# Kernel optimization log

Measured on AMD Instinct MI355X. Metric: run time of the kernel, lower is better.

## Reference

```python
import jax, jax.numpy as jnp
import numpy as np

HID = 64
NUM_LAYERS = 2
EPS = 1e-5


def _layernorm(x, g, b):
    mu = jnp.mean(x, axis=-1, keepdims=True)
    var = jnp.mean(jnp.square(x - mu), axis=-1, keepdims=True)
    return (x - mu) * jax.lax.rsqrt(var + EPS) * g + b


def _mlp(x, w1, b1, g, beta, w2, b2):
    # Linear -> LayerNorm -> ReLU -> Linear (torch Linear: x @ W.T + b)
    h = x @ w1.T + b1
    h = jax.nn.relu(_layernorm(h, g, beta))
    return h @ w2.T + b2


def _gru(x, h, wih, whh, bih, bhh):
    # PyTorch GRUCell semantics
    gi = x @ wih.T + bih
    gh = h @ whh.T + bhh
    ir, iz, inn = jnp.split(gi, 3, axis=-1)
    hr, hz, hn = jnp.split(gh, 3, axis=-1)
    r = jax.nn.sigmoid(ir + hr)
    z = jax.nn.sigmoid(iz + hz)
    n = jnp.tanh(inn + r * hn)
    return (1.0 - z) * n + z * h


def setup_inputs() -> dict:
    key = jax.random.key(0)
    ks = iter(jax.random.split(key, 64))
    s = 0.05

    def rn(shape):
        return jax.random.normal(next(ks), shape, dtype=jnp.float32) * s

    B, M, K1 = 32, 256, 128
    inp = {
        'hybrid_input': jax.random.normal(next(ks), (B, M, K1, 4), dtype=jnp.float32),
        'hidden_state': jnp.zeros((B, HID), dtype=jnp.float32),
        # input encoder
        'enc_w1': rn((HID, 4)), 'enc_b1': rn((HID,)),
        'enc_g': jnp.ones((HID,), jnp.float32), 'enc_beta': jnp.zeros((HID,), jnp.float32),
        'enc_w2': rn((HID, HID)), 'enc_b2': rn((HID,)),
        # per-layer, per-side (axis0=layer, axis1=[row,col]) params
        'l_w1': rn((NUM_LAYERS, 2, HID, HID)), 'l_b1': rn((NUM_LAYERS, 2, HID)),
        'l_g': jnp.ones((NUM_LAYERS, 2, HID), jnp.float32), 'l_beta': jnp.zeros((NUM_LAYERS, 2, HID), jnp.float32),
        'l_w2': rn((NUM_LAYERS, 2, HID, HID)), 'l_b2': rn((NUM_LAYERS, 2, HID)),
        'l_gwih': rn((NUM_LAYERS, 2, 3 * HID, HID)), 'l_gwhh': rn((NUM_LAYERS, 2, 3 * HID, HID)),
        'l_gbih': rn((NUM_LAYERS, 2, 3 * HID)), 'l_gbhh': rn((NUM_LAYERS, 2, 3 * HID)),
        # top-level GRU
        'g_wih': rn((3 * HID, HID)), 'g_whh': rn((3 * HID, HID)),
        'g_bih': rn((3 * HID,)), 'g_bhh': rn((3 * HID,)),
        # head: Linear(2H->H) -> ReLU -> Linear(H->1)
        'head_w1': rn((HID, 2 * HID)), 'head_b1': rn((HID,)),
        'head_w2': rn((1, HID)), 'head_b2': rn((1,)),
    }
    return inp


def reference(hybrid_input, hidden_state, enc_w1, enc_b1, enc_g, enc_beta, enc_w2, enc_b2,
              l_w1, l_b1, l_g, l_beta, l_w2, l_b2, l_gwih, l_gwhh, l_gbih, l_gbhh,
              g_wih, g_whh, g_bih, g_bhh, head_w1, head_b1, head_w2, head_b2):
    # input encoder
    x = _mlp(hybrid_input, enc_w1, enc_b1, enc_g, enc_beta, enc_w2, enc_b2)

    for l in range(NUM_LAYERS):
        # row pass: max over axis 2 (K+1)
        row_max = jnp.max(x, axis=2, keepdims=True)
        upd = _mlp(x - row_max, l_w1[l, 0], l_b1[l, 0], l_g[l, 0], l_beta[l, 0], l_w2[l, 0], l_b2[l, 0])
        x = _gru(upd, x, l_gwih[l, 0], l_gwhh[l, 0], l_gbih[l, 0], l_gbhh[l, 0])
        # col pass: max over axis 1 (M)
        col_max = jnp.max(x, axis=1, keepdims=True)
        upd = _mlp(x - col_max, l_w1[l, 1], l_b1[l, 1], l_g[l, 1], l_beta[l, 1], l_w2[l, 1], l_b2[l, 1])
        x = _gru(upd, x, l_gwih[l, 1], l_gwhh[l, 1], l_gbih[l, 1], l_gbhh[l, 1])

    B, M, K1, h = x.shape
    global_feat = jnp.max(x.reshape(B, M * K1, h), axis=1)  # (B, H)
    new_hidden = _gru(global_feat, hidden_state, g_wih, g_whh, g_bih, g_bhh)

    h_exp = jnp.broadcast_to(new_hidden[:, None, None, :], (B, M, K1, h))
    combined = jnp.concatenate([x, h_exp], axis=-1)  # (B, M, K1, 2H)
    hh = jax.nn.relu(combined @ head_w1.T + head_b1)
    logits = (hh @ head_w2.T + head_b2)[..., 0]  # (B, M, K1)
    return logits, new_hidden
```

## Files before the change

kernel.cpp:

```cpp
#include <hip/hip_runtime.h>
#include <math.h>

typedef unsigned int u32;
typedef unsigned short u16;
typedef __attribute__((ext_vector_type(4))) float f32x4;
typedef __attribute__((ext_vector_type(8))) short s16x8;

#define NTOT 1048576
#define SWZ(n, col) ((col) ^ (((n) & 7) << 4))

__device__ __forceinline__ float bflo(u32 v) { return __uint_as_float(v << 16); }
__device__ __forceinline__ float bfhi(u32 v) { return __uint_as_float(v & 0xffff0000u); }
__device__ __forceinline__ u32 rndbf(float f) {
  u32 u = __float_as_uint(f);
  return u + 0x7fffu + ((u >> 16) & 1u);
}
__device__ __forceinline__ u32 pk2(float a, float b) {
  return __builtin_amdgcn_perm(rndbf(b), rndbf(a), 0x07060302u);
}
__device__ __forceinline__ float sigm(float x) {
  return __builtin_amdgcn_rcpf(1.0f + __expf(-x));
}
__device__ __forceinline__ float tanh_f(float x) {
  float e = __expf(2.0f * x);
  return 1.0f - 2.0f * __builtin_amdgcn_rcpf(e + 1.0f);
}
__device__ __forceinline__ float relu(float x) { return fmaxf(x, 0.0f); }

__device__ __forceinline__ void gemmG(const ushort* __restrict__ gA,
                                      const unsigned char* L, int boff,
                                      int ws, int l, int lq, int lr,
                                      f32x4 acc[4]) {
  s16x8 a0 = *(const s16x8*)(gA + ((ws * 128 + l) << 3));
  s16x8 a1 = *(const s16x8*)(gA + ((ws * 128 + 64 + l) << 3));
  const int c0 = (lq << 4) ^ ((lr & 7) << 4);
  const unsigned char* Bp = L + boff + lr * 128;
#pragma unroll
  for (int nt = 0; nt < 4; ++nt) {
    s16x8 b0 = *(const s16x8*)(Bp + nt * 2048 + c0);
    s16x8 b1 = *(const s16x8*)(Bp + nt * 2048 + (c0 ^ 64));
    acc[nt] = __builtin_amdgcn_mfma_f32_16x16x32_bf16(a0, b0, acc[nt], 0, 0, 0);
    acc[nt] = __builtin_amdgcn_mfma_f32_16x16x32_bf16(a1, b1, acc[nt], 0, 0, 0);
  }
}

__device__ __forceinline__ void gemmG2(const ushort* __restrict__ gA,
                                       const unsigned char* L, int boff,
                                       int ws, int nh, int l, int lq, int lr,
                                       f32x4 acc[4]) {
  s16x8 a0 = *(const s16x8*)(gA + ((ws * 128 + l) << 3));
  s16x8 a1 = *(const s16x8*)(gA + ((ws * 128 + 64 + l) << 3));
  const int c0 = (lq << 4) ^ ((lr & 7) << 4);
  const unsigned char* Bp = L + boff + nh * 8192 + lr * 128;
#pragma unroll
  for (int nt = 0; nt < 4; ++nt) {
    s16x8 b0 = *(const s16x8*)(Bp + nt * 2048 + c0);
    s16x8 b1 = *(const s16x8*)(Bp + nt * 2048 + (c0 ^ 64));
    acc[nt] = __builtin_amdgcn_mfma_f32_16x16x32_bf16(a0, b0, acc[nt], 0, 0, 0);
    acc[nt] = __builtin_amdgcn_mfma_f32_16x16x32_bf16(a1, b1, acc[nt], 0, 0, 0);
  }
}

__device__ __forceinline__ void binit(f32x4 acc[4], float x, float y, float z, float w) {
  f32x4 v; v[0] = x; v[1] = y; v[2] = z; v[3] = w;
#pragma unroll
  for (int nt = 0; nt < 4; ++nt) acc[nt] = v;
}

__global__ void diag_kernel(float* out, float v) { out[0] = v; }

__global__ __launch_bounds__(256) void prep_kernel(
    const float* __restrict__ enc_w2, const float* __restrict__ head_w1,
    const float* __restrict__ l_w1, const float* __restrict__ l_w2,
    const float* __restrict__ l_gwih, const float* __restrict__ l_gwhh,
    ushort* __restrict__ gwF) {
  const int id = blockIdx.x;
  const int t = threadIdx.x;
  const float* src;
  int ld = 64;
  if (id == 0)      { src = enc_w2; }
  else if (id == 1) { src = head_w1; ld = 128; }
  else if (id < 6)  { src = l_w1 + (id - 2) * 4096; }
  else if (id < 10) { src = l_w2 + (id - 6) * 4096; }
  else if (id < 22) { int q = id - 10; src = l_gwih + (q / 3) * 12288 + (q % 3) * 4096; }
  else              { int q = id - 22; src = l_gwhh + (q / 3) * 12288 + (q % 3) * 4096; }
  uint4* dst = (uint4*)(gwF + (size_t)id * 4096);
#pragma unroll
  for (int i = 0; i < 2; ++i) {
    int ch = i * 256 + t;
    int q = ch & 63;
    int g = ch >> 6;
    int j = (g >> 1) * 16 + (q & 15);
    int k = (g & 1) * 32 + (q >> 4) * 8;
    const float* s = src + (size_t)j * ld + k;
    float4 f0 = *(const float4*)(s);
    float4 f1 = *(const float4*)(s + 4);
    uint4 o;
    o.x = pk2(f0.x, f0.y); o.y = pk2(f0.z, f0.w);
    o.z = pk2(f1.x, f1.y); o.w = pk2(f1.z, f1.w);
    dst[ch] = o;
  }
}

__global__ __launch_bounds__(512) void encoder_kernel(
    const float4* __restrict__ hyb, ushort* __restrict__ xG,
    const ushort* __restrict__ gwF, const float* __restrict__ enc_w1,
    const float* __restrict__ b1, const float* __restrict__ gg,
    const float* __restrict__ be, const float* __restrict__ b2,
    float* __restrict__ rmOut) {
  __shared__ __align__(16) unsigned char L[17920];
  const int t = threadIdx.x;
  const int w = t >> 6, l = t & 63, lq = l >> 4, lr = l & 15;
  const int ws = w & 3, nh = w >> 2;
  const int gbase = blockIdx.x * 128;
  const int j0 = ws * 16 + lq * 4;

  if (t < 256) ((float*)(L + 16384))[t] = enc_w1[t];
  __syncthreads();

  {
    const int n = t >> 2, part = t & 3;
    float4 iv = hyb[gbase + n];
    const float* W1 = (const float*)(L + 16384);
    float h[16];
#pragma unroll
    for (int jj = 0; jj < 16; ++jj) {
      int j = part * 16 + jj;
      float4 wr = *(const float4*)(W1 + j * 4);
      h[jj] = b1[j] + wr.x * iv.x + wr.y * iv.y + wr.z * iv.z + wr.w * iv.w;
    }
    float s = 0.f, q = 0.f;
#pragma unroll
    for (int jj = 0; jj < 16; ++jj) { s += h[jj]; q += h[jj] * h[jj]; }
    s += __shfl_xor(s, 1); q += __shfl_xor(q, 1);
    s += __shfl_xor(s, 2); q += __shfl_xor(q, 2);
    float mean = s * (1.f / 64.f);
    float rstd = rsqrtf(q * (1.f / 64.f) - mean * mean + 1e-5f);
    u32 pk[8];
#pragma unroll
    for (int jj = 0; jj < 16; jj += 2) {
      int j = part * 16 + jj;
      float v0 = relu((h[jj] - mean) * rstd * gg[j] + be[j]);
      float v1 = relu((h[jj + 1] - mean) * rstd * gg[j + 1] + be[j + 1]);
      pk[jj >> 1] = pk2(v0, v1);
    }
    *(uint4*)(L + n * 128 + SWZ(n, part * 32))      = make_uint4(pk[0], pk[1], pk[2], pk[3]);
    *(uint4*)(L + n * 128 + SWZ(n, part * 32 + 16)) = make_uint4(pk[4], pk[5], pk[6], pk[7]);
  }
  __syncthreads();

  float4 vb2 = *(const float4*)(b2 + j0);
  f32x4 acc[4];
  binit(acc, vb2.x, vb2.y, vb2.z, vb2.w);
  gemmG2(gwF, L, 0, ws, nh, l, lq, lr, acc);
  {
    ushort* xout = xG + (size_t)gbase * 64;
#pragma unroll
    for (int nt = 0; nt < 4; ++nt) {
      int n = nh * 64 + nt * 16 + lr;
      *(uint2*)(xout + (size_t)n * 64 + j0) =
          make_uint2(pk2(acc[nt][0], acc[nt][1]), pk2(acc[nt][2], acc[nt][3]));
    }
  }
  {
    float mt[4];
#pragma unroll
    for (int r = 0; r < 4; ++r)
      mt[r] = fmaxf(fmaxf(acc[0][r], acc[1][r]), fmaxf(acc[2][r], acc[3][r]));
#pragma unroll
    for (int m = 1; m < 16; m <<= 1)
#pragma unroll
      for (int r = 0; r < 4; ++r) mt[r] = fmaxf(mt[r], __shfl_xor(mt[r], m));
    if (lr == 0) {
      float4 v; v.x = mt[0]; v.y = mt[1]; v.z = mt[2]; v.w = mt[3];
      *(float4*)(L + 17408 + (nh * 64 + j0) * 4) = v;
    }
  }
  __syncthreads();
  if (t < 64) {
    const float* R = (const float*)(L + 17408);
    float v = fmaxf(R[t], R[64 + t]);
    rmOut[(size_t)(blockIdx.x * 2 + 0) * 64 + t] = v;
    rmOut[(size_t)(blockIdx.x * 2 + 1) * 64 + t] = v;
  }
}

#define PXL 0
#define PP  8192
#define PMV 16384
#define PU  16384
#define PRED 24576

__global__ __launch_bounds__(256, 5) void pass_kernel(
    ushort* __restrict__ xG, const ushort* __restrict__ gwF,
    const float* __restrict__ rmP, const ushort* __restrict__ cmB, int mode,
    int s_w1, int s_w2, int s_ih0, int s_hh0,
    const float* __restrict__ b1, const float* __restrict__ b2,
    const float* __restrict__ gg, const float* __restrict__ be,
    const float* __restrict__ bih, const float* __restrict__ bhh,
    float* __restrict__ rmOut) {
  __shared__ __align__(16) unsigned char L[26624];
  const int t = threadIdx.x;
  const int ws = t >> 6, l = t & 63, lq = l >> 4, lr = l & 15;
  const int gbase = blockIdx.x * 64;
  const int j0 = ws * 16 + lq * 4;
  const int colb = ws * 32 + lq * 8;
  const int rowp = (gbase >> 7) * 2;
  const int b = gbase >> 15;
  const int k1b = gbase & 127;

  const ushort* Aw1 = gwF + (size_t)s_w1 * 4096;
  const ushort* Aw2 = gwF + (size_t)s_w2 * 4096;
  const ushort* Ai0 = gwF + (size_t)s_ih0 * 4096;
  const ushort* Ai1 = Ai0 + 4096;
  const ushort* Ai2 = Ai1 + 4096;
  const ushort* Ah0 = gwF + (size_t)s_hh0 * 4096;
  const ushort* Ah1 = Ah0 + 4096;
  const ushort* Ah2 = Ah1 + 4096;

  {
    const uint4* xrow = (const uint4*)(xG + (size_t)gbase * 64);
    const int c = t & 7;
    uint4 mvo;
    if (mode == 0) {
      const float* r0 = rmP + (size_t)rowp * 64 + c * 8;
      float mv[8];
#pragma unroll
      for (int q = 0; q < 8; ++q) mv[q] = -fmaxf(r0[q], r0[64 + q]);
      mvo.x = pk2(mv[0], mv[1]); mvo.y = pk2(mv[2], mv[3]);
      mvo.z = pk2(mv[4], mv[5]); mvo.w = pk2(mv[6], mv[7]);
    }
#pragma unroll
    for (int i = 0; i < 2; ++i) {
      int flat = i * 256 + t; int n = flat >> 3;
      *(uint4*)(L + PXL + n * 128 + SWZ(n, c * 16)) = xrow[(size_t)n * 8 + c];
      uint4 o = mvo;
      if (mode == 1)
        o = ((const uint4*)cmB)[(size_t)(b * 128 + k1b + n) * 8 + c];
      *(uint4*)(L + PMV + n * 128 + SWZ(n, c * 16)) = o;
    }
  }
  __syncthreads();

  f32x4 acc[4];
  { float4 v = *(const float4*)(b1 + j0); binit(acc, v.x, v.y, v.z, v.w); }
  gemmG(Aw1, L, PXL, ws, l, lq, lr, acc);
  gemmG(Aw1, L, PMV, ws, l, lq, lr, acc);
#pragma unroll
  for (int nt = 0; nt < 4; ++nt) {
    float s = acc[nt][0] + acc[nt][1] + acc[nt][2] + acc[nt][3];
    float q = acc[nt][0] * acc[nt][0] + acc[nt][1] * acc[nt][1] +
              acc[nt][2] * acc[nt][2] + acc[nt][3] * acc[nt][3];
    s += __shfl_xor(s, 16); q += __shfl_xor(q, 16);
    s += __shfl_xor(s, 32); q += __shfl_xor(q, 32);
    if (lq == 0)
      *(float2*)(L + PRED + (ws * 64 + nt * 16 + lr) * 8) = make_float2(s, q);
  }
  __syncthreads();
  {
    float4 vg = *(const float4*)(gg + j0);
    float4 vbe = *(const float4*)(be + j0);
    float gv[4] = {vg.x, vg.y, vg.z, vg.w};
    float bv[4] = {vbe.x, vbe.y, vbe.z, vbe.w};
#pragma unroll
    for (int nt = 0; nt < 4; ++nt) {
      int np = nt * 16 + lr;
      float ss = 0.f, qq = 0.f;
#pragma unroll
      for (int wv = 0; wv < 4; ++wv) {
        float2 pr = *(const float2*)(L + PRED + (wv * 64 + np) * 8);
        ss += pr.x; qq += pr.y;
      }
      float mean = ss * (1.f / 64.f);
      float rstd = rsqrtf(qq * (1.f / 64.f) - mean * mean + 1e-5f);
      float h_[4];
#pragma unroll
      for (int r = 0; r < 4; ++r) h_[r] = relu((acc[nt][r] - mean) * rstd * gv[r] + bv[r]);
      *(uint2*)(L + PP + np * 128 + SWZ(np, colb)) =
          make_uint2(pk2(h_[0], h_[1]), pk2(h_[2], h_[3]));
    }
  }
  __syncthreads();
  __builtin_amdgcn_sched_barrier(0);

  { float4 v = *(const float4*)(b2 + j0); binit(acc, v.x, v.y, v.z, v.w); }
  gemmG(Aw2, L, PP, ws, l, lq, lr, acc);
#pragma unroll
  for (int nt = 0; nt < 4; ++nt) {
    int n = nt * 16 + lr;
    *(uint2*)(L + PU + n * 128 + SWZ(n, colb)) =
        make_uint2(pk2(acc[nt][0], acc[nt][1]), pk2(acc[nt][2], acc[nt][3]));
  }
  __builtin_amdgcn_sched_barrier(0);

  f32x4 ah[4];
  { float4 v = *(const float4*)(bhh + 128 + j0); binit(ah, v.x, v.y, v.z, v.w); }
  gemmG(Ah2, L, PXL, ws, l, lq, lr, ah);
  __syncthreads();
  __builtin_amdgcn_sched_barrier(0);

  f32x4 ar[4];
  { float4 vi = *(const float4*)(bih + j0);
    float4 vh = *(const float4*)(bhh + j0);
    binit(ar, vi.x + vh.x, vi.y + vh.y, vi.z + vh.z, vi.w + vh.w); }
  gemmG(Ai0, L, PU, ws, l, lq, lr, ar);
  gemmG(Ah0, L, PXL, ws, l, lq, lr, ar);
  __builtin_amdgcn_sched_barrier(0);

  f32x4 an[4];
  { float4 v = *(const float4*)(bih + 128 + j0);
    float bv[4] = {v.x, v.y, v.z, v.w};
#pragma unroll
    for (int nt = 0; nt < 4; ++nt)
#pragma unroll
      for (int r = 0; r < 4; ++r)
        an[nt][r] = bv[r] + sigm(ar[nt][r]) * ah[nt][r];
  }
  gemmG(Ai2, L, PU, ws, l, lq, lr, an);
  __builtin_amdgcn_sched_barrier(0);

  f32x4 az[4];
  { float4 vi = *(const float4*)(bih + 64 + j0);
    float4 vh = *(const float4*)(bhh + 64 + j0);
    binit(az, vi.x + vh.x, vi.y + vh.y, vi.z + vh.z, vi.w + vh.w); }
  gemmG(Ai1, L, PU, ws, l, lq, lr, az);
  gemmG(Ah1, L, PXL, ws, l, lq, lr, az);

  float xn[4][4];
#pragma unroll
  for (int nt = 0; nt < 4; ++nt) {
    int n = nt * 16 + lr;
    uint2 xo = *(const uint2*)(L + PXL + n * 128 + SWZ(n, colb));
    float xv[4] = {bflo(xo.x), bfhi(xo.x), bflo(xo.y), bfhi(xo.y)};
#pragma unroll
    for (int r = 0; r < 4; ++r) {
      float nn = tanh_f(an[nt][r]);
      float zz = sigm(az[nt][r]);
      xn[nt][r] = nn + zz * (xv[r] - nn);
    }
  }
  {
    ushort* xout = xG + (size_t)gbase * 64;
#pragma unroll
    for (int nt = 0; nt < 4; ++nt) {
      int n = nt * 16 + lr;
      *(uint2*)(xout + (size_t)n * 64 + j0) =
          make_uint2(pk2(xn[nt][0], xn[nt][1]), pk2(xn[nt][2], xn[nt][3]));
    }
  }
  {
    float mt[4];
#pragma unroll
    for (int r = 0; r < 4; ++r)
      mt[r] = fmaxf(fmaxf(xn[0][r], xn[1][r]), fmaxf(xn[2][r], xn[3][r]));
#pragma unroll
    for (int m = 1; m < 16; m <<= 1)
#pragma unroll
      for (int r = 0; r < 4; ++r) mt[r] = fmaxf(mt[r], __shfl_xor(mt[r], m));
    if (lr == 0) {
      float4 v; v.x = mt[0]; v.y = mt[1]; v.z = mt[2]; v.w = mt[3];
      *(float4*)(rmOut + (size_t)blockIdx.x * 64 + j0) = v;
    }
  }
}

__global__ __launch_bounds__(256) void colmax_kernel(const ushort* __restrict__ xG,
                                                     ushort* __restrict__ cmB) {
  const int t = threadIdx.x;
  const int b = blockIdx.x >> 4, kg = blockIdx.x & 15;
  const int col = t & 31, k1 = kg * 8 + (t >> 5);
  const u32* xu = (const u32*)xG;
  float m0 = -INFINITY, m1 = -INFINITY;
  for (int m = 0; m < 256; ++m) {
    size_t node = ((size_t)(b * 256 + m)) * 128 + k1;
    u32 v = xu[node * 32 + col];
    m0 = fmaxf(m0, bflo(v)); m1 = fmaxf(m1, bfhi(v));
  }
  ((u32*)cmB)[((size_t)(b * 128 + k1)) * 32 + col] = pk2(-m0, -m1);
}

__global__ __launch_bounds__(64) void topgru_kernel(
    const float* __restrict__ rm, const float* __restrict__ hs,
    const float* __restrict__ gwih, const float* __restrict__ gwhh,
    const float* __restrict__ gbih, const float* __restrict__ gbhh,
    float* __restrict__ nh, float* __restrict__ outTail) {
  __shared__ float gf[64], h0[64];
  const int b = blockIdx.x, j = threadIdx.x;
  float g0 = -INFINITY, g1 = -INFINITY, g2 = -INFINITY, g3 = -INFINITY;
  const float* base = rm + (size_t)b * 512 * 64 + j;
  for (int r = 0; r < 512; r += 4) {
    g0 = fmaxf(g0, base[(r + 0) * 64]);
    g1 = fmaxf(g1, base[(r + 1) * 64]);
    g2 = fmaxf(g2, base[(r + 2) * 64]);
    g3 = fmaxf(g3, base[(r + 3) * 64]);
  }
  gf[j] = fmaxf(fmaxf(g0, g1), fmaxf(g2, g3));
  h0[j] = hs[b * 64 + j];
  __syncthreads();
  float gi[3], gh[3];
#pragma unroll
  for (int g = 0; g < 3; ++g) {
    float s = gbih[g * 64 + j];
    const float* wr = gwih + (g * 64 + j) * 64;
    for (int k = 0; k < 64; ++k) s += wr[k] * gf[k];
    gi[g] = s;
  }
#pragma unroll
  for (int g = 0; g < 3; ++g) {
    float s = gbhh[g * 64 + j];
    const float* wr = gwhh + (g * 64 + j) * 64;
    for (int k = 0; k < 64; ++k) s += wr[k] * h0[k];
    gh[g] = s;
  }
  float rr = sigm(gi[0] + gh[0]);
  float zz = sigm(gi[1] + gh[1]);
  float nn = tanh_f(gi[2] + rr * gh[2]);
  float val = (1.0f - zz) * nn + zz * h0[j];
  nh[b * 64 + j] = val;
  outTail[b * 64 + j] = val;
}

__global__ __launch_bounds__(64) void hc_kernel(const float* __restrict__ nh,
                                                const float* __restrict__ hw1,
                                                const float* __restrict__ hb1,
                                                float* __restrict__ hc) {
  __shared__ float h0[64];
  const int b = blockIdx.x, j = threadIdx.x;
  h0[j] = nh[b * 64 + j];
  __syncthreads();
  float s = hb1[j];
  const float* wr = hw1 + j * 128 + 64;
  for (int k = 0; k < 64; ++k) s += wr[k] * h0[k];
  hc[b * 64 + j] = s;
}

__global__ __launch_bounds__(512) void head_kernel(
    const ushort* __restrict__ xG, const ushort* __restrict__ gwF,
    const float* __restrict__ hc, const float* __restrict__ hw2,
    const float* __restrict__ hb2, float* __restrict__ out) {
  __shared__ __align__(16) unsigned char L[18432];
  const int t = threadIdx.x;
  const int w = t >> 6, l = t & 63, lq = l >> 4, lr = l & 15;
  const int ws = w & 3, nh = w >> 2;
  const int gbase = blockIdx.x * 128;
  const int b = gbase >> 15;
  const int j0 = ws * 16 + lq * 4;

  { const uint4* xrow = (const uint4*)(xG + (size_t)gbase * 64);
#pragma unroll
    for (int i = 0; i < 2; ++i) {
      int flat = i * 512 + t; int n = flat >> 3, c = flat & 7;
      *(uint4*)(L + n * 128 + SWZ(n, c * 16)) = xrow[(size_t)n * 8 + c];
    } }
  __syncthreads();

  float4 vhc = *(const float4*)(hc + b * 64 + j0);
  f32x4 acc[4];
  binit(acc, vhc.x, vhc.y, vhc.z, vhc.w);
  gemmG2(gwF + 4096, L, 0, ws, nh, l, lq, lr, acc);

  float4 w2v = *(const float4*)(hw2 + j0);
  float w2a[4] = {w2v.x, w2v.y, w2v.z, w2v.w};
#pragma unroll
  for (int nt = 0; nt < 4; ++nt) {
    float p = 0.f;
#pragma unroll
    for (int r = 0; r < 4; ++r) p += w2a[r] * relu(acc[nt][r]);
    p += __shfl_xor(p, 16);
    p += __shfl_xor(p, 32);
    if (lq == 0) ((float*)(L + 16384))[(nh * 4 + ws) * 64 + nt * 16 + lr] = p;
  }
  __syncthreads();
  if (t < 128) {
    const float* red = (const float*)(L + 16384) + (t >> 6) * 256 + (t & 63);
    out[gbase + t] = red[0] + red[64] + red[128] + red[192] + hb2[0];
  }
}

extern "C" void kernel_launch(void* const* d_in, const int* in_sizes, int n_in,
                              void* d_out, int out_size, void* d_ws, size_t ws_size,
                              hipStream_t stream) {
  const float* hybrid   = (const float*)d_in[0];
  const float* hidden   = (const float*)d_in[1];
  const float* enc_w1   = (const float*)d_in[2];
  const float* enc_b1   = (const float*)d_in[3];
  const float* enc_g    = (const float*)d_in[4];
  const float* enc_beta = (const float*)d_in[5];
  const float* enc_w2   = (const float*)d_in[6];
  const float* enc_b2   = (const float*)d_in[7];
  const float* l_w1     = (const float*)d_in[8];
  const float* l_b1     = (const float*)d_in[9];
  const float* l_g      = (const float*)d_in[10];
  const float* l_beta   = (const float*)d_in[11];
  const float* l_w2     = (const float*)d_in[12];
  const float* l_b2     = (const float*)d_in[13];
  const float* l_gwih   = (const float*)d_in[14];
  const float* l_gwhh   = (const float*)d_in[15];
  const float* l_gbih   = (const float*)d_in[16];
  const float* l_gbhh   = (const float*)d_in[17];
  const float* g_wih    = (const float*)d_in[18];
  const float* g_whh    = (const float*)d_in[19];
  const float* g_bih    = (const float*)d_in[20];
  const float* g_bhh    = (const float*)d_in[21];
  const float* head_w1  = (const float*)d_in[22];
  const float* head_b1  = (const float*)d_in[23];
  const float* head_w2  = (const float*)d_in[24];
  const float* head_b2  = (const float*)d_in[25];

  char* p = (char*)d_ws;
  size_t off = 0;
  auto carve = [&](size_t bytes) { void* r = p + off; off = (off + bytes + 255) & ~255ULL; return r; };
  ushort* xG  = (ushort*)carve((size_t)NTOT * 64 * 2);
  ushort* gwF = (ushort*)carve(34 * 4096 * 2);
  float*  rmA = (float*)carve((size_t)16384 * 64 * 4);
  float*  rmB = (float*)carve((size_t)16384 * 64 * 4);
  ushort* cmB = (ushort*)carve((size_t)32 * 128 * 64 * 2);
  float*  nh  = (float*)carve(2048 * 4);
  float*  hcb = (float*)carve(2048 * 4);

  if (ws_size < off) {
    diag_kernel<<<1, 1, 0, stream>>>((float*)d_out, 1.0f + (float)ws_size * 1e-9f);
    return;
  }

  prep_kernel<<<34, 256, 0, stream>>>(enc_w2, head_w1, l_w1, l_w2, l_gwih, l_gwhh, gwF);
  encoder_kernel<<<8192, 512, 0, stream>>>((const float4*)hybrid, xG, gwF, enc_w1,
                                           enc_b1, enc_g, enc_beta, enc_b2, rmA);

  float* rmRead = rmA;
  float* rmWrite = rmB;
  for (int lyr = 0; lyr < 2; ++lyr) {
    for (int s = 0; s < 2; ++s) {
      const int m = lyr * 2 + s;
      if (s == 1) colmax_kernel<<<512, 256, 0, stream>>>(xG, cmB);
      pass_kernel<<<16384, 256, 0, stream>>>(
          xG, gwF, rmRead, cmB, s,
          2 + m, 6 + m, 10 + 3 * m, 22 + 3 * m,
          l_b1 + m * 64, l_b2 + m * 64, l_g + m * 64, l_beta + m * 64,
          l_gbih + m * 192, l_gbhh + m * 192, rmWrite);
      float* tmp = rmRead; rmRead = rmWrite; rmWrite = tmp;
    }
  }

  topgru_kernel<<<32, 64, 0, stream>>>(rmRead, hidden, g_wih, g_whh, g_bih, g_bhh,
                                       nh, (float*)d_out + 1048576);
  hc_kernel<<<32, 64, 0, stream>>>(nh, head_w1, head_b1, hcb);
  head_kernel<<<8192, 512, 0, stream>>>(xG, gwF, hcb, head_w2, head_b2, (float*)d_out);
}
```

Baseline: 764.2 us.

## Load MFMA B operands from global into registers instead of staging through LDS

The pass and head kernels now read x fragments straight from global memory into per-lane registers in MFMA B-operand layout and reuse them across the W1 and the three GRU hidden GEMMs, instead of staging x (and the max vector) in swizzled LDS. In row mode the broadcast row-max term is reduced to a single MFMA pair instead of a full 64-column GEMM, since all columns share the same vector. This cuts LDS use per block (the pass kernel's launch bound drops from 5 to 4 blocks per SIMD) and removes a staging barrier. The cost is more VGPR pressure, and the final GRU blend rereads x from global.

```diff
diff --git a/kernel.cpp b/kernel.cpp
--- a/kernel.cpp
+++ b/kernel.cpp
@@ -18,6 +18,12 @@
 __device__ __forceinline__ u32 pk2(float a, float b) {
   return __builtin_amdgcn_perm(rndbf(b), rndbf(a), 0x07060302u);
 }
+__device__ __forceinline__ s16x8 pack8(const float m[8]) {
+  union { u32 w[4]; s16x8 v; } cv;
+  cv.w[0] = pk2(m[0], m[1]); cv.w[1] = pk2(m[2], m[3]);
+  cv.w[2] = pk2(m[4], m[5]); cv.w[3] = pk2(m[6], m[7]);
+  return cv.v;
+}
 __device__ __forceinline__ float sigm(float x) {
   return __builtin_amdgcn_rcpf(1.0f + __expf(-x));
 }
@@ -26,6 +32,18 @@
   return 1.0f - 2.0f * __builtin_amdgcn_rcpf(e + 1.0f);
 }
 __device__ __forceinline__ float relu(float x) { return fmaxf(x, 0.0f); }
+
+__device__ __forceinline__ void gemmR(const ushort* __restrict__ gA,
+                                      const s16x8 bf[8],
+                                      int ws, int l, f32x4 acc[4]) {
+  s16x8 a0 = *(const s16x8*)(gA + ((ws * 128 + l) << 3));
+  s16x8 a1 = *(const s16x8*)(gA + ((ws * 128 + 64 + l) << 3));
+#pragma unroll
+  for (int nt = 0; nt < 4; ++nt) {
+    acc[nt] = __builtin_amdgcn_mfma_f32_16x16x32_bf16(a0, bf[nt * 2 + 0], acc[nt], 0, 0, 0);
+    acc[nt] = __builtin_amdgcn_mfma_f32_16x16x32_bf16(a1, bf[nt * 2 + 1], acc[nt], 0, 0, 0);
+  }
+}
 
 __device__ __forceinline__ void gemmG(const ushort* __restrict__ gA,
                                       const unsigned char* L, int boff,
@@ -35,23 +53,6 @@
   s16x8 a1 = *(const s16x8*)(gA + ((ws * 128 + 64 + l) << 3));
   const int c0 = (lq << 4) ^ ((lr & 7) << 4);
   const unsigned char* Bp = L + boff + lr * 128;
-#pragma unroll
-  for (int nt = 0; nt < 4; ++nt) {
-    s16x8 b0 = *(const s16x8*)(Bp + nt * 2048 + c0);
-    s16x8 b1 = *(const s16x8*)(Bp + nt * 2048 + (c0 ^ 64));
-    acc[nt] = __builtin_amdgcn_mfma_f32_16x16x32_bf16(a0, b0, acc[nt], 0, 0, 0);
-    acc[nt] = __builtin_amdgcn_mfma_f32_16x16x32_bf16(a1, b1, acc[nt], 0, 0, 0);
-  }
-}
-
-__device__ __forceinline__ void gemmG2(const ushort* __restrict__ gA,
-                                       const unsigned char* L, int boff,
-                                       int ws, int nh, int l, int lq, int lr,
-                                       f32x4 acc[4]) {
-  s16x8 a0 = *(const s16x8*)(gA + ((ws * 128 + l) << 3));
-  s16x8 a1 = *(const s16x8*)(gA + ((ws * 128 + 64 + l) << 3));
-  const int c0 = (lq << 4) ^ ((lr & 7) << 4);
-  const unsigned char* Bp = L + boff + nh * 8192 + lr * 128;
 #pragma unroll
   for (int nt = 0; nt < 4; ++nt) {
     s16x8 b0 = *(const s16x8*)(Bp + nt * 2048 + c0);
@@ -152,7 +153,19 @@
   float4 vb2 = *(const float4*)(b2 + j0);
   f32x4 acc[4];
   binit(acc, vb2.x, vb2.y, vb2.z, vb2.w);
-  gemmG2(gwF, L, 0, ws, nh, l, lq, lr, acc);
+  {
+    s16x8 a0 = *(const s16x8*)(gwF + ((ws * 128 + l) << 3));
+    s16x8 a1 = *(const s16x8*)(gwF + ((ws * 128 + 64 + l) << 3));
+    const int c0 = (lq << 4) ^ ((lr & 7) << 4);
+    const unsigned char* Bp = L + nh * 8192 + lr * 128;
+#pragma unroll
+    for (int nt = 0; nt < 4; ++nt) {
+      s16x8 b0 = *(const s16x8*)(Bp + nt * 2048 + c0);
+      s16x8 b1 = *(const s16x8*)(Bp + nt * 2048 + (c0 ^ 64));
+      acc[nt] = __builtin_amdgcn_mfma_f32_16x16x32_bf16(a0, b0, acc[nt], 0, 0, 0);
+      acc[nt] = __builtin_amdgcn_mfma_f32_16x16x32_bf16(a1, b1, acc[nt], 0, 0, 0);
+    }
+  }
   {
     ushort* xout = xG + (size_t)gbase * 64;
 #pragma unroll
@@ -185,13 +198,11 @@
   }
 }
 
-#define PXL 0
-#define PP  8192
-#define PMV 16384
-#define PU  16384
-#define PRED 24576
-
-__global__ __launch_bounds__(256, 5) void pass_kernel(
+#define PP  0
+#define PU  8192
+#define PRED 16384
+
+__global__ __launch_bounds__(256, 4) void pass_kernel(
     ushort* __restrict__ xG, const ushort* __restrict__ gwF,
     const float* __restrict__ rmP, const ushort* __restrict__ cmB, int mode,
     int s_w1, int s_w2, int s_ih0, int s_hh0,
@@ -199,7 +210,7 @@
     const float* __restrict__ gg, const float* __restrict__ be,
     const float* __restrict__ bih, const float* __restrict__ bhh,
     float* __restrict__ rmOut) {
-  __shared__ __align__(16) unsigned char L[26624];
+  __shared__ __align__(16) unsigned char L[18432];
   const int t = threadIdx.x;
   const int ws = t >> 6, l = t & 63, lq = l >> 4, lr = l & 15;
   const int gbase = blockIdx.x * 64;
@@ -218,34 +229,51 @@
   const ushort* Ah1 = Ah0 + 4096;
   const ushort* Ah2 = Ah1 + 4096;
 
-  {
-    const uint4* xrow = (const uint4*)(xG + (size_t)gbase * 64);
-    const int c = t & 7;
-    uint4 mvo;
+  s16x8 bx[8];
+  {
+    const ushort* xp = xG + ((size_t)(gbase + lr)) * 64 + lq * 8;
+#pragma unroll
+    for (int nt = 0; nt < 4; ++nt) {
+      bx[nt * 2 + 0] = *(const s16x8*)(xp + nt * 1024);
+      bx[nt * 2 + 1] = *(const s16x8*)(xp + nt * 1024 + 32);
+    }
+  }
+
+  f32x4 acc[4];
+  {
+    float4 vb1 = *(const float4*)(b1 + j0);
     if (mode == 0) {
-      const float* r0 = rmP + (size_t)rowp * 64 + c * 8;
-      float mv[8];
-#pragma unroll
-      for (int q = 0; q < 8; ++q) mv[q] = -fmaxf(r0[q], r0[64 + q]);
-      mvo.x = pk2(mv[0], mv[1]); mvo.y = pk2(mv[2], mv[3]);
-      mvo.z = pk2(mv[4], mv[5]); mvo.w = pk2(mv[6], mv[7]);
-    }
-#pragma unroll
-    for (int i = 0; i < 2; ++i) {
-      int flat = i * 256 + t; int n = flat >> 3;
-      *(uint4*)(L + PXL + n * 128 + SWZ(n, c * 16)) = xrow[(size_t)n * 8 + c];
-      uint4 o = mvo;
-      if (mode == 1)
-        o = ((const uint4*)cmB)[(size_t)(b * 128 + k1b + n) * 8 + c];
-      *(uint4*)(L + PMV + n * 128 + SWZ(n, c * 16)) = o;
-    }
-  }
-  __syncthreads();
-
-  f32x4 acc[4];
-  { float4 v = *(const float4*)(b1 + j0); binit(acc, v.x, v.y, v.z, v.w); }
-  gemmG(Aw1, L, PXL, ws, l, lq, lr, acc);
-  gemmG(Aw1, L, PMV, ws, l, lq, lr, acc);
+      float m0[8], m1[8];
+      const float* r0 = rmP + (size_t)rowp * 64;
+#pragma unroll
+      for (int q = 0; q < 8; ++q) {
+        m0[q] = -fmaxf(r0[lq * 8 + q], r0[64 + lq * 8 + q]);
+        m1[q] = -fmaxf(r0[32 + lq * 8 + q], r0[96 + lq * 8 + q]);
+      }
+      s16x8 bmv0 = pack8(m0), bmv1 = pack8(m1);
+      s16x8 a0 = *(const s16x8*)(Aw1 + ((ws * 128 + l) << 3));
+      s16x8 a1 = *(const s16x8*)(Aw1 + ((ws * 128 + 64 + l) << 3));
+      f32x4 dmv; dmv[0] = 0.f; dmv[1] = 0.f; dmv[2] = 0.f; dmv[3] = 0.f;
+      dmv = __builtin_amdgcn_mfma_f32_16x16x32_bf16(a0, bmv0, dmv, 0, 0, 0);
+      dmv = __builtin_amdgcn_mfma_f32_16x16x32_bf16(a1, bmv1, dmv, 0, 0, 0);
+#pragma unroll
+      for (int nt = 0; nt < 4; ++nt) {
+        acc[nt][0] = vb1.x + dmv[0]; acc[nt][1] = vb1.y + dmv[1];
+        acc[nt][2] = vb1.z + dmv[2]; acc[nt][3] = vb1.w + dmv[3];
+      }
+    } else {
+      binit(acc, vb1.x, vb1.y, vb1.z, vb1.w);
+      s16x8 bmv[8];
+      const ushort* cp = cmB + ((size_t)(b * 128 + k1b + lr)) * 64 + lq * 8;
+#pragma unroll
+      for (int nt = 0; nt < 4; ++nt) {
+        bmv[nt * 2 + 0] = *(const s16x8*)(cp + nt * 1024);
+        bmv[nt * 2 + 1] = *(const s16x8*)(cp + nt * 1024 + 32);
+      }
+      gemmR(Aw1, bmv, ws, l, acc);
+    }
+  }
+  gemmR(Aw1, bx, ws, l, acc);
 #pragma unroll
   for (int nt = 0; nt < 4; ++nt) {
     float s = acc[nt][0] + acc[nt][1] + acc[nt][2] + acc[nt][3];
@@ -295,7 +323,7 @@
 
   f32x4 ah[4];
   { float4 v = *(const float4*)(bhh + 128 + j0); binit(ah, v.x, v.y, v.z, v.w); }
-  gemmG(Ah2, L, PXL, ws, l, lq, lr, ah);
+  gemmR(Ah2, bx, ws, l, ah);
   __syncthreads();
   __builtin_amdgcn_sched_barrier(0);
 
@@ -304,7 +332,7 @@
     float4 vh = *(const float4*)(bhh + j0);
     binit(ar, vi.x + vh.x, vi.y + vh.y, vi.z + vh.z, vi.w + vh.w); }
   gemmG(Ai0, L, PU, ws, l, lq, lr, ar);
-  gemmG(Ah0, L, PXL, ws, l, lq, lr, ar);
+  gemmR(Ah0, bx, ws, l, ar);
   __builtin_amdgcn_sched_barrier(0);
 
   f32x4 an[4];
@@ -324,13 +352,13 @@
     float4 vh = *(const float4*)(bhh + 64 + j0);
     binit(az, vi.x + vh.x, vi.y + vh.y, vi.z + vh.z, vi.w + vh.w); }
   gemmG(Ai1, L, PU, ws, l, lq, lr, az);
-  gemmG(Ah1, L, PXL, ws, l, lq, lr, az);
+  gemmR(Ah1, bx, ws, l, az);
 
   float xn[4][4];
 #pragma unroll
   for (int nt = 0; nt < 4; ++nt) {
     int n = nt * 16 + lr;
-    uint2 xo = *(const uint2*)(L + PXL + n * 128 + SWZ(n, colb));
+    uint2 xo = *(const uint2*)(xG + ((size_t)(gbase + n)) * 64 + j0);
     float xv[4] = {bflo(xo.x), bfhi(xo.x), bflo(xo.y), bfhi(xo.y)};
 #pragma unroll
     for (int r = 0; r < 4; ++r) {
@@ -438,7 +466,7 @@
     const ushort* __restrict__ xG, const ushort* __restrict__ gwF,
     const float* __restrict__ hc, const float* __restrict__ hw2,
     const float* __restrict__ hb2, float* __restrict__ out) {
-  __shared__ __align__(16) unsigned char L[18432];
+  __shared__ float RED[512];
   const int t = threadIdx.x;
   const int w = t >> 6, l = t & 63, lq = l >> 4, lr = l & 15;
   const int ws = w & 3, nh = w >> 2;
@@ -446,18 +474,19 @@
   const int b = gbase >> 15;
   const int j0 = ws * 16 + lq * 4;
 
-  { const uint4* xrow = (const uint4*)(xG + (size_t)gbase * 64);
-#pragma unroll
-    for (int i = 0; i < 2; ++i) {
-      int flat = i * 512 + t; int n = flat >> 3, c = flat & 7;
-      *(uint4*)(L + n * 128 + SWZ(n, c * 16)) = xrow[(size_t)n * 8 + c];
-    } }
-  __syncthreads();
-
+  s16x8 bh[8];
+  {
+    const ushort* xp = xG + ((size_t)(gbase + nh * 64 + lr)) * 64 + lq * 8;
+#pragma unroll
+    for (int nt = 0; nt < 4; ++nt) {
+      bh[nt * 2 + 0] = *(const s16x8*)(xp + nt * 1024);
+      bh[nt * 2 + 1] = *(const s16x8*)(xp + nt * 1024 + 32);
+    }
+  }
   float4 vhc = *(const float4*)(hc + b * 64 + j0);
   f32x4 acc[4];
   binit(acc, vhc.x, vhc.y, vhc.z, vhc.w);
-  gemmG2(gwF + 4096, L, 0, ws, nh, l, lq, lr, acc);
+  gemmR(gwF + 4096, bh, ws, l, acc);
 
   float4 w2v = *(const float4*)(hw2 + j0);
   float w2a[4] = {w2v.x, w2v.y, w2v.z, w2v.w};
@@ -468,11 +497,11 @@
     for (int r = 0; r < 4; ++r) p += w2a[r] * relu(acc[nt][r]);
     p += __shfl_xor(p, 16);
     p += __shfl_xor(p, 32);
-    if (lq == 0) ((float*)(L + 16384))[(nh * 4 + ws) * 64 + nt * 16 + lr] = p;
+    if (lq == 0) RED[(nh * 4 + ws) * 64 + nt * 16 + lr] = p;
   }
   __syncthreads();
   if (t < 128) {
-    const float* red = (const float*)(L + 16384) + (t >> 6) * 256 + (t & 63);
+    const float* red = RED + (t >> 6) * 256 + (t & 63);
     out[gbase + t] = red[0] + red[64] + red[128] + red[192] + hb2[0];
   }
 }
```

Result: slower. 1.004 ms (+31.4%).
